# Optimization experiments

Measured on AMD Instinct MI355X. Metric: run time of the kernel, lower is better.

The kernel has to match this reference:

```python
import jax, jax.numpy as jnp
import numpy as np

B, L1, L2, C = 8, 2048, 2048, 320
H, D = 8, 64            # heads, dim_head -> inner_dim = 512
NREG = 4                # num_register_tokens
INNER = H * D
SCALE = D ** -0.5


def setup_inputs() -> dict:
    key = jax.random.key(0)
    ks = jax.random.split(key, 9)
    x = jax.random.normal(ks[0], (B, L1, C), dtype=jnp.float32)
    context = jax.random.normal(ks[1], (B, L2, C), dtype=jnp.float32)
    attn_mask = jax.random.randint(ks[2], (B, L1, L2), 0, 2).astype(bool)
    s = C ** -0.5
    Wq = jax.random.normal(ks[3], (C, INNER), dtype=jnp.float32) * s
    Wk = jax.random.normal(ks[4], (C, INNER), dtype=jnp.float32) * s
    Wv = jax.random.normal(ks[5], (C, INNER), dtype=jnp.float32) * s
    Wo = jax.random.normal(ks[6], (INNER, C), dtype=jnp.float32) * (INNER ** -0.5)
    bo = jnp.zeros((C,), dtype=jnp.float32)
    reg_tokens = jax.random.normal(ks[7], (1, NREG, C), dtype=jnp.float32)
    return {"x": x, "context": context, "attn_mask": attn_mask,
            "Wq": Wq, "Wk": Wk, "Wv": Wv, "Wo": Wo, "bo": bo,
            "reg_tokens": reg_tokens}


def reference(x, context, attn_mask, Wq, Wk, Wv, Wo, bo, reg_tokens):
    b = x.shape[0]
    # prepend register tokens to context: [B, NREG+L2, C]
    ctx = jnp.concatenate([jnp.broadcast_to(reg_tokens, (b, NREG, C)), context], axis=1)
    q = (x @ Wq).reshape(b, L1, H, D).transpose(0, 2, 1, 3)          # B H L1 D
    k = (ctx @ Wk).reshape(b, NREG + L2, H, D).transpose(0, 2, 1, 3)  # B H Lk D
    v = (ctx @ Wv).reshape(b, NREG + L2, H, D).transpose(0, 2, 1, 3)
    # pad mask with True for register tokens (always visible)
    mask = jnp.pad(attn_mask, ((0, 0), (0, 0), (NREG, 0)), constant_values=True)
    scores = jnp.einsum('bhqd,bhkd->bhqk', q, k) * SCALE              # B H L1 Lk
    scores = jnp.where(mask[:, None, :, :], scores, -jnp.inf)
    attn = jax.nn.softmax(scores, axis=-1)
    out = jnp.einsum('bhqk,bhkd->bhqd', attn, v)                      # B H L1 D
    out = out.transpose(0, 2, 1, 3).reshape(b, L1, INNER)             # B L1 (H D)
    return out @ Wo + bo
```

## Files before the change

kernel.cpp:

```cpp
#include <hip/hip_runtime.h>
#include <hip/hip_bf16.h>

#define B_ 8
#define L1_ 2048
#define L2_ 2048
#define C_ 320
#define H_ 8
#define D_ 64
#define NREG_ 4
#define INNER_ 512
#define LK_ 2052
#define LKP_ 2112
#define NKV_TILES 33
#define LOG2E 1.44269504f
#define QSCALE (0.125f * LOG2E)

typedef __bf16 bf16_t;
typedef __attribute__((ext_vector_type(8))) __bf16 bf16x8;
typedef __attribute__((ext_vector_type(4))) __bf16 bf16x4;
typedef __attribute__((ext_vector_type(4))) float f32x4;

__device__ __forceinline__ f32x4 mfma16(bf16x8 a, bf16x8 b, f32x4 c){
  return __builtin_amdgcn_mfma_f32_16x16x32_bf16(a, b, c, 0, 0, 0);
}

__device__ __forceinline__ void gl_lds16(const char* g, char* l){
  __builtin_amdgcn_global_load_lds(
      (const __attribute__((address_space(1))) unsigned int*)g,
      (__attribute__((address_space(3))) unsigned int*)l, 16, 0, 0);
}

__device__ __forceinline__ float fexp2(float x){
  float r; asm("v_exp_f32 %0, %1" : "=v"(r) : "v"(x)); return r;
}

__device__ __forceinline__ int swzK(int row){ return (row & 3) | ((row >> 1) & 4); }
__device__ __forceinline__ int swzV(int row){ return row & 7; }

__global__ void k_transpose(const float* __restrict__ Wq, const float* __restrict__ Wk,
                            const float* __restrict__ Wv, const float* __restrict__ Wo,
                            bf16_t* __restrict__ Wqt, bf16_t* __restrict__ Wkt,
                            bf16_t* __restrict__ Wvt, bf16_t* __restrict__ Wot){
  int z = blockIdx.z;
  int K = (z < 3) ? C_ : INNER_;
  int N = (z < 3) ? INNER_ : C_;
  if (blockIdx.x * 32 >= N || blockIdx.y * 32 >= K) return;
  const float* W = (z == 0) ? Wq : (z == 1) ? Wk : (z == 2) ? Wv : Wo;
  bf16_t* Wt = (z == 0) ? Wqt : (z == 1) ? Wkt : (z == 2) ? Wvt : Wot;
  float sc = (z == 0) ? QSCALE : 1.0f;
  __shared__ float t[32][33];
  int n0 = blockIdx.x * 32, k0 = blockIdx.y * 32;
  int tx = threadIdx.x & 31, ty = threadIdx.x >> 5;
  for (int r = ty; r < 32; r += 8) t[r][tx] = W[(long)(k0 + r) * N + n0 + tx];
  __syncthreads();
  for (int r = ty; r < 32; r += 8) Wt[(long)(n0 + r) * K + k0 + tx] = (bf16_t)(t[tx][r] * sc);
}

__global__ __launch_bounds__(256)
void k_cvt(const float* __restrict__ x, const float* __restrict__ ctx,
           const float* __restrict__ regt,
           bf16_t* __restrict__ xb, bf16_t* __restrict__ ctxb){
  long g = (long)blockIdx.x * 256 + threadIdx.x;
  if (blockIdx.y == 0){
    if (g >= (long)16384 * 80) return;
    f32x4 v = *(const f32x4*)(x + g * 4);
    bf16x4 cv;
    cv[0]=(bf16_t)v[0]; cv[1]=(bf16_t)v[1]; cv[2]=(bf16_t)v[2]; cv[3]=(bf16_t)v[3];
    *(bf16x4*)(xb + g * 4) = cv;
  } else {
    if (g >= (long)16896 * 80) return;
    long row = g / 80;
    int col = (int)(g - row * 80) * 4;
    int b = (int)(row / LKP_);
    int rr = (int)(row - (long)b * LKP_);
    f32x4 v = (f32x4){0,0,0,0};
    if (rr < NREG_)    v = *(const f32x4*)(regt + rr * C_ + col);
    else if (rr < LK_) v = *(const f32x4*)(ctx + ((long)(b * L1_ + rr - NREG_)) * C_ + col);
    bf16x4 cv;
    cv[0]=(bf16_t)v[0]; cv[1]=(bf16_t)v[1]; cv[2]=(bf16_t)v[2]; cv[3]=(bf16_t)v[3];
    *(bf16x4*)(ctxb + row * C_ + col) = cv;
  }
}

__global__ void k_maskcompact(const void* __restrict__ maskv,
                              unsigned int* __restrict__ maskp){
  int row = blockIdx.x * 4 + (threadIdx.x >> 6);
  int l = threadIdx.x & 63;
  const unsigned char* mb = (const unsigned char*)maskv;
  const int* mi = (const int*)maskv;
  int bad = 0;
  #pragma unroll
  for (int jj = 0; jj < 4; jj++){
    int j = l + jj * 64;
    if ((j & 3) != 0 && mb[j] != 0) bad = 1;
  }
  int isInt = (__ballot(bad) == 0ull) ? 1 : 0;
  unsigned int* orow = maskp + (long)row * 66;
  if (!isInt){
    const unsigned char* rp = mb + (long)row * L2_;
    unsigned wdv = 0;
    #pragma unroll
    for (int i = 0; i < 8; i++){
      unsigned u;
      if (l == 0 && i == 0) u = 0x01010101u;
      else u = *(const unsigned*)(rp + (32 * l - 4 + 4 * i));
      unsigned bits = 0;
      bits |= (u & 0x000000FFu) ? 1u : 0u;
      bits |= (u & 0x0000FF00u) ? 2u : 0u;
      bits |= (u & 0x00FF0000u) ? 4u : 0u;
      bits |= (u & 0xFF000000u) ? 8u : 0u;
      wdv |= bits << (4 * i);
    }
    orow[l] = wdv;
    if (l < 2){
      unsigned wd2 = 0;
      if (l == 0){
        unsigned u = *(const unsigned*)(rp + 2044);
        wd2 |= (u & 0x000000FFu) ? 1u : 0u;
        wd2 |= (u & 0x0000FF00u) ? 2u : 0u;
        wd2 |= (u & 0x00FF0000u) ? 4u : 0u;
        wd2 |= (u & 0xFF000000u) ? 8u : 0u;
      }
      orow[64 + l] = wd2;
    }
  } else {
    long base = (long)row * L2_;
    for (int s = 0; s < 33; s++){
      int kv = s * 64 + l;
      int vis = 0;
      if (kv < NREG_) vis = 1;
      else if (kv < LK_) vis = (mi[base + kv - NREG_] != 0);
      unsigned long long bal = __ballot(vis);
      if (l == 0)      orow[2*s]   = (unsigned int)bal;
      else if (l == 1) orow[2*s+1] = (unsigned int)(bal >> 32);
    }
  }
}

__global__ __launch_bounds__(256)
void k_proj(const bf16_t* __restrict__ xb, const bf16_t* __restrict__ ctxb,
            const bf16_t* __restrict__ Wqt, const bf16_t* __restrict__ Wkt,
            const bf16_t* __restrict__ Wvt,
            bf16_t* __restrict__ Qw, bf16_t* __restrict__ Kw, bf16_t* __restrict__ Vtw)
{
  int mode = blockIdx.z;
  if (mode == 0 && blockIdx.x >= 128) return;
  const char* Ab = (const char*)((mode == 0) ? xb : ctxb);
  const char* Wtb = (const char*)((mode == 0) ? Wqt : (mode == 1) ? Wkt : Wvt);
  bf16_t* out = (mode == 0) ? Qw : (mode == 1) ? Kw : Vtw;

  __shared__ __align__(16) char As[128*64*2];
  __shared__ __align__(16) char Bs[128*64*2];
  int tid = threadIdx.x;
  int w = tid >> 6, lane = tid & 63, cl = lane & 15, cg = lane >> 4;
  int wr = w >> 1, wc = w & 1;
  int m0 = blockIdx.x * 128, n0 = blockIdx.y * 128;

  f32x4 acc[4][4];
  #pragma unroll
  for (int i = 0; i < 4; i++)
    #pragma unroll
    for (int j = 0; j < 4; j++) acc[i][j] = (f32x4){0,0,0,0};

  for (int kb = 0; kb < 5; ++kb){
    __syncthreads();
    #pragma unroll
    for (int c = 0; c < 4; c++){
      int e = c * 4096 + tid * 16;
      int row = e >> 7, irb = e & 127;
      gl_lds16(Ab + (long)(m0 + row) * 640 + kb * 128 + (irb ^ ((row & 7) << 4)), As + e);
    }
    #pragma unroll
    for (int c = 0; c < 4; c++){
      int e = c * 4096 + tid * 16;
      int row = e >> 7, irb = e & 127;
      gl_lds16(Wtb + (long)(n0 + row) * 640 + kb * 128 + (irb ^ ((row & 7) << 4)), Bs + e);
    }
    asm volatile("s_waitcnt vmcnt(0)" ::: "memory");
    __syncthreads();
    #pragma unroll
    for (int kc = 0; kc < 2; kc++){
      int kk = kc * 32 + cg * 8;
      bf16x8 af[4], bfr[4];
      #pragma unroll
      for (int mt = 0; mt < 4; mt++){
        int row = wr * 64 + mt * 16 + cl;
        af[mt] = *(const bf16x8*)(As + (row << 7) + ((kk << 1) ^ ((row & 7) << 4)));
      }
      #pragma unroll
      for (int nt = 0; nt < 4; nt++){
        int row = wc * 64 + nt * 16 + cl;
        bfr[nt] = *(const bf16x8*)(Bs + (row << 7) + ((kk << 1) ^ ((row & 7) << 4)));
      }
      #pragma unroll
      for (int mt = 0; mt < 4; mt++)
        #pragma unroll
        for (int nt = 0; nt < 4; nt++)
          acc[mt][nt] = mfma16(af[mt], bfr[nt], acc[mt][nt]);
    }
  }

  #pragma unroll
  for (int mt = 0; mt < 4; mt++){
    #pragma unroll
    for (int nt = 0; nt < 4; nt++){
      f32x4 v = acc[mt][nt];
      int row = m0 + wr * 64 + mt * 16 + cg * 4;
      int col = n0 + wc * 64 + nt * 16 + cl;
      int h = col >> 6, d = col & 63;
      if (mode == 0){
        int b = row >> 11, l1 = row & 2047;
        bf16_t* p = out + ((long)((b * H_ + h) * L1_ + l1)) * D_ + d;
        #pragma unroll
        for (int r = 0; r < 4; r++) p[r * D_] = (bf16_t)v[r];
      } else if (mode == 1){
        int b = row / LKP_, rr = row - b * LKP_;
        bf16_t* p = out + ((long)((b * H_ + h) * LKP_ + rr)) * D_ + d;
        #pragma unroll
        for (int r = 0; r < 4; r++) p[r * D_] = (bf16_t)v[r];
      } else {
        int b = row / LKP_, rr = row - b * LKP_;
        bf16x4 cv;
        cv[0]=(bf16_t)v[0]; cv[1]=(bf16_t)v[1]; cv[2]=(bf16_t)v[2]; cv[3]=(bf16_t)v[3];
        *(bf16x4*)(out + ((long)((b * H_ + h) * D_ + d)) * LKP_ + rr) = cv;
      }
    }
  }
}

__global__ __launch_bounds__(512)
void k_attn(const bf16_t* __restrict__ Q, const bf16_t* __restrict__ K,
            const bf16_t* __restrict__ Vt, const unsigned int* __restrict__ maskp,
            bf16_t* __restrict__ att)
{
  __shared__ __align__(16) char smem[32768];
  int lin = blockIdx.x;
  int xcd = lin & 7, idx = lin >> 3;
  int bh = xcd * 8 + (idx >> 3);
  int qb = idx & 7;
  const int b = bh >> 3, h = bh & 7;
  const int tid = threadIdx.x, w = tid >> 6, lane = tid & 63;
  const int cl = lane & 15, cg = lane >> 4;
  const int qw = qb * 256 + w * 32;

  const char* Kg = (const char*)(K + (long)bh * LKP_ * D_);
  const char* Vg = (const char*)(Vt + (long)bh * D_ * LKP_);

  bf16x8 qf[2][2];
  const unsigned int* mrow[2];
  #pragma unroll
  for (int qg = 0; qg < 2; qg++){
    const bf16_t* Qb = Q + ((long)bh * L1_ + qw + qg*16 + cl) * D_;
    qf[qg][0] = *(const bf16x8*)(Qb + cg*8);
    qf[qg][1] = *(const bf16x8*)(Qb + 32 + cg*8);
    mrow[qg] = maskp + (long)(b * L1_ + qw + qg*16 + cl) * 66;
  }

  bf16x8 ones8;
  #pragma unroll
  for (int i = 0; i < 8; i++) ones8[i] = (bf16_t)1.0f;

  f32x4 o[2][4];
  f32x4 sacc[2];
  #pragma unroll
  for (int qg = 0; qg < 2; qg++){
    sacc[qg] = (f32x4){0,0,0,0};
    #pragma unroll
    for (int dt = 0; dt < 4; dt++) o[qg][dt] = (f32x4){0,0,0,0};
  }

  const int sp = tid * 16;
  const int srow = sp >> 7, sir = sp & 127;
  const int kgo = (srow << 7) + (sir ^ (swzK(srow) << 4));
  const long vgo = (long)srow * (LKP_ * 2) + (sir ^ (swzV(srow) << 4));

  gl_lds16(Kg + kgo, smem + sp);
  gl_lds16(Vg + vgo, smem + 16384 + sp);
  uint2 wd_cur[2];
  #pragma unroll
  for (int qg = 0; qg < 2; qg++) wd_cur[qg] = *(const uint2*)(mrow[qg]);
  asm volatile("s_waitcnt vmcnt(0)" ::: "memory");
  __syncthreads();

  for (int t = 0; t < NKV_TILES; ++t){
    int tn = (t + 1 < NKV_TILES) ? t + 1 : NKV_TILES - 1;
    gl_lds16(Kg + (long)tn * 8192 + kgo, smem + ((t + 1) & 1) * 8192 + sp);
    gl_lds16(Vg + vgo + tn * 128, smem + 16384 + ((t + 1) & 1) * 8192 + sp);
    uint2 wd_nxt[2];
    #pragma unroll
    for (int qg = 0; qg < 2; qg++) wd_nxt[qg] = *(const uint2*)(mrow[qg] + 2*tn);

    const char* Kb = smem + (t & 1) * 8192;
    const char* Vb = smem + 16384 + (t & 1) * 8192;

    f32x4 s[2][4];
    __builtin_amdgcn_s_setprio(1);
    #pragma unroll
    for (int T = 0; T < 4; T++){
      int row = 32*(T>>1) + 8*(cl>>2) + 4*(T&1) + (cl&3);
      int sw = swzK(row) << 4;
      const char* rp = Kb + (row << 7);
      bf16x8 kf0 = *(const bf16x8*)(rp + ((16*cg) ^ sw));
      bf16x8 kf1 = *(const bf16x8*)(rp + ((64 + 16*cg) ^ sw));
      #pragma unroll
      for (int qg = 0; qg < 2; qg++){
        f32x4 z = (f32x4){0,0,0,0};
        z = mfma16(kf0, qf[qg][0], z);
        z = mfma16(kf1, qf[qg][1], z);
        s[qg][T] = z;
      }
    }
    __builtin_amdgcn_s_setprio(0);

    bf16x8 pa[2][2];
    #pragma unroll
    for (int qg = 0; qg < 2; qg++){
      #pragma unroll
      for (int T = 0; T < 4; T++){
        unsigned wsel = (T < 2) ? wd_cur[qg].x : wd_cur[qg].y;
        unsigned nib = (wsel >> (8*cg + 4*(T&1))) & 0xFu;
        float p0 = fexp2(s[qg][T][0]);
        float p1 = fexp2(s[qg][T][1]);
        float p2 = fexp2(s[qg][T][2]);
        float p3 = fexp2(s[qg][T][3]);
        p0 = (nib & 1u) ? p0 : 0.f;
        p1 = (nib & 2u) ? p1 : 0.f;
        p2 = (nib & 4u) ? p2 : 0.f;
        p3 = (nib & 8u) ? p3 : 0.f;
        int a = T >> 1, jb = (T & 1) * 4;
        pa[qg][a][jb+0] = (bf16_t)p0;
        pa[qg][a][jb+1] = (bf16_t)p1;
        pa[qg][a][jb+2] = (bf16_t)p2;
        pa[qg][a][jb+3] = (bf16_t)p3;
      }
    }

    __builtin_amdgcn_s_setprio(1);
    #pragma unroll
    for (int qg = 0; qg < 2; qg++){
      sacc[qg] = mfma16(ones8, pa[qg][0], sacc[qg]);
      sacc[qg] = mfma16(ones8, pa[qg][1], sacc[qg]);
    }
    #pragma unroll
    for (int dt = 0; dt < 4; dt++){
      int row = 16*dt + cl;
      int sw = swzV(row) << 4;
      const char* rp = Vb + (row << 7);
      bf16x8 vf0 = *(const bf16x8*)(rp + ((16*cg) ^ sw));
      bf16x8 vf1 = *(const bf16x8*)(rp + ((64 + 16*cg) ^ sw));
      #pragma unroll
      for (int qg = 0; qg < 2; qg++){
        o[qg][dt] = mfma16(pa[qg][0], vf0, o[qg][dt]);
        o[qg][dt] = mfma16(pa[qg][1], vf1, o[qg][dt]);
      }
    }
    __builtin_amdgcn_s_setprio(0);

    asm volatile("s_waitcnt vmcnt(0)" ::: "memory");
    __syncthreads();
    wd_cur[0] = wd_nxt[0];
    wd_cur[1] = wd_nxt[1];
  }

  #pragma unroll
  for (int qg = 0; qg < 2; qg++){
    float inv = 1.0f / sacc[qg][0];
    float ir0 = __shfl(inv, (lane & 48) | (cg*4 + 0));
    float ir1 = __shfl(inv, (lane & 48) | (cg*4 + 1));
    float ir2 = __shfl(inv, (lane & 48) | (cg*4 + 2));
    float ir3 = __shfl(inv, (lane & 48) | (cg*4 + 3));
    int qbase = qw + qg*16 + cg*4;
    #pragma unroll
    for (int dt = 0; dt < 4; dt++){
      bf16_t* op = att + ((long)(b * L1_) + qbase) * INNER_ + h * D_ + 16*dt + cl;
      op[0] = (bf16_t)(o[qg][dt][0] * ir0);
      op[INNER_] = (bf16_t)(o[qg][dt][1] * ir1);
      op[2*INNER_] = (bf16_t)(o[qg][dt][2] * ir2);
      op[3*INNER_] = (bf16_t)(o[qg][dt][3] * ir3);
    }
  }
}

__global__ __launch_bounds__(256)
void k_out(const bf16_t* __restrict__ A, const bf16_t* __restrict__ Wot,
           const float* __restrict__ bo, float* __restrict__ out)
{
  __shared__ __align__(16) char As[128*64*2];
  __shared__ __align__(16) char Bs[64*64*2];
  int tid = threadIdx.x;
  int w = tid >> 6, lane = tid & 63, cl = lane & 15, cg = lane >> 4;
  int wr = w >> 1, wc = w & 1;
  int m0 = blockIdx.x * 128, n0 = blockIdx.y * 64;
  const char* Ab = (const char*)A;
  const char* Bb = (const char*)Wot;

  f32x4 acc[4][2];
  #pragma unroll
  for (int i = 0; i < 4; i++)
    #pragma unroll
    for (int j = 0; j < 2; j++) acc[i][j] = (f32x4){0,0,0,0};

  for (int kb = 0; kb < 8; kb++){
    __syncthreads();
    #pragma unroll
    for (int c = 0; c < 4; c++){
      int e = c * 4096 + tid * 16;
      int row = e >> 7, irb = e & 127;
      gl_lds16(Ab + (long)(m0 + row) * 1024 + kb * 128 + (irb ^ ((row & 7) << 4)), As + e);
    }
    #pragma unroll
    for (int c = 0; c < 2; c++){
      int e = c * 4096 + tid * 16;
      int row = e >> 7, irb = e & 127;
      gl_lds16(Bb + (long)(n0 + row) * 1024 + kb * 128 + (irb ^ ((row & 7) << 4)), Bs + e);
    }
    asm volatile("s_waitcnt vmcnt(0)" ::: "memory");
    __syncthreads();
    #pragma unroll
    for (int kc = 0; kc < 2; kc++){
      int kk = kc * 32 + cg * 8;
      bf16x8 af[4], bfr[2];
      #pragma unroll
      for (int mt = 0; mt < 4; mt++){
        int row = wr * 64 + mt * 16 + cl;
        af[mt] = *(const bf16x8*)(As + (row << 7) + ((kk << 1) ^ ((row & 7) << 4)));
      }
      #pragma unroll
      for (int nt = 0; nt < 2; nt++){
        int row = wc * 32 + nt * 16 + cl;
        bfr[nt] = *(const bf16x8*)(Bs + (row << 7) + ((kk << 1) ^ ((row & 7) << 4)));
      }
      #pragma unroll
      for (int mt = 0; mt < 4; mt++)
        #pragma unroll
        for (int nt = 0; nt < 2; nt++)
          acc[mt][nt] = mfma16(af[mt], bfr[nt], acc[mt][nt]);
    }
  }
  #pragma unroll
  for (int mt = 0; mt < 4; mt++)
    #pragma unroll
    for (int nt = 0; nt < 2; nt++){
      int row = m0 + wr * 64 + mt * 16 + cg * 4;
      int col = n0 + wc * 32 + nt * 16 + cl;
      float bias = bo[col];
      #pragma unroll
      for (int r = 0; r < 4; r++)
        out[(long)(row + r) * C_ + col] = acc[mt][nt][r] + bias;
    }
}

extern "C" void kernel_launch(void* const* d_in, const int* in_sizes, int n_in,
                              void* d_out, int out_size, void* d_ws, size_t ws_size,
                              hipStream_t stream)
{
  const float* x    = (const float*)d_in[0];
  const float* ctx  = (const float*)d_in[1];
  const void*  mask = d_in[2];
  const float* Wq   = (const float*)d_in[3];
  const float* Wk   = (const float*)d_in[4];
  const float* Wv   = (const float*)d_in[5];
  const float* Wo   = (const float*)d_in[6];
  const float* bo   = (const float*)d_in[7];
  const float* regt = (const float*)d_in[8];
  float* out = (float*)d_out;

  char* ws = (char*)d_ws;
  size_t off = 256;
  unsigned int* maskp = (unsigned int*)(ws + off);    off += (size_t)16384 * 66 * 4;
  bf16_t* Qw  = (bf16_t*)(ws + off);                  off += (size_t)B_*H_*L1_*D_*2;
  bf16_t* Kw  = (bf16_t*)(ws + off);                  off += (size_t)B_*H_*LKP_*D_*2;
  bf16_t* Vtw = (bf16_t*)(ws + off);                  off += (size_t)B_*H_*D_*LKP_*2;
  size_t Roff = off;
  bf16_t* xb   = (bf16_t*)(ws + Roff);
  bf16_t* ctxb = (bf16_t*)(ws + Roff + (size_t)16384*C_*2);
  bf16_t* Att  = (bf16_t*)(ws + Roff);
  off = Roff + (size_t)16384*C_*2 + (size_t)16896*C_*2;
  bf16_t* Wqt = (bf16_t*)(ws + off);                  off += (size_t)C_*INNER_*2;
  bf16_t* Wkt = (bf16_t*)(ws + off);                  off += (size_t)C_*INNER_*2;
  bf16_t* Wvt = (bf16_t*)(ws + off);                  off += (size_t)C_*INNER_*2;
  bf16_t* Wot = (bf16_t*)(ws + off);                  off += (size_t)C_*INNER_*2;
  (void)ws_size; (void)in_sizes; (void)n_in; (void)out_size;

  k_transpose<<<dim3(16,16,4), 256, 0, stream>>>(Wq, Wk, Wv, Wo, Wqt, Wkt, Wvt, Wot);
  k_cvt<<<dim3(5280,2), 256, 0, stream>>>(x, ctx, regt, xb, ctxb);
  k_maskcompact<<<4096, 256, 0, stream>>>(mask, maskp);
  k_proj<<<dim3(132,4,3), 256, 0, stream>>>(xb, ctxb, Wqt, Wkt, Wvt, Qw, Kw, Vtw);
  k_attn<<<512, 512, 0, stream>>>(Qw, Kw, Vtw, maskp, Att);
  k_out<<<dim3(128,5), 256, 0, stream>>>(Att, Wot, bo, out);
}
```

Measured before the change: 206.1 us.

## Fuse prep kernels into one launch and double-buffer projection GEMM loads

Merges the weight transpose, input conversion and mask compaction kernels into a single launch that dispatches on block index, removing two kernel launches and their inter-kernel gaps. The projection and output GEMMs now use double-buffered LDS: each iteration prefetches the next K tile with global_load_lds while computing on the current one, with partial vmcnt waits and an extra barrier. This doubles LDS use per block, which may lower occupancy, and the shared-memory transpose tile is now allocated for every block of the fused kernel.

```diff
diff --git a/kernel.cpp b/kernel.cpp
--- a/kernel.cpp
+++ b/kernel.cpp
@@ -37,102 +37,104 @@
 __device__ __forceinline__ int swzK(int row){ return (row & 3) | ((row >> 1) & 4); }
 __device__ __forceinline__ int swzV(int row){ return row & 7; }
 
-__global__ void k_transpose(const float* __restrict__ Wq, const float* __restrict__ Wk,
-                            const float* __restrict__ Wv, const float* __restrict__ Wo,
-                            bf16_t* __restrict__ Wqt, bf16_t* __restrict__ Wkt,
-                            bf16_t* __restrict__ Wvt, bf16_t* __restrict__ Wot){
-  int z = blockIdx.z;
-  int K = (z < 3) ? C_ : INNER_;
-  int N = (z < 3) ? INNER_ : C_;
-  if (blockIdx.x * 32 >= N || blockIdx.y * 32 >= K) return;
-  const float* W = (z == 0) ? Wq : (z == 1) ? Wk : (z == 2) ? Wv : Wo;
-  bf16_t* Wt = (z == 0) ? Wqt : (z == 1) ? Wkt : (z == 2) ? Wvt : Wot;
-  float sc = (z == 0) ? QSCALE : 1.0f;
-  __shared__ float t[32][33];
-  int n0 = blockIdx.x * 32, k0 = blockIdx.y * 32;
-  int tx = threadIdx.x & 31, ty = threadIdx.x >> 5;
-  for (int r = ty; r < 32; r += 8) t[r][tx] = W[(long)(k0 + r) * N + n0 + tx];
-  __syncthreads();
-  for (int r = ty; r < 32; r += 8) Wt[(long)(n0 + r) * K + k0 + tx] = (bf16_t)(t[tx][r] * sc);
-}
-
 __global__ __launch_bounds__(256)
-void k_cvt(const float* __restrict__ x, const float* __restrict__ ctx,
-           const float* __restrict__ regt,
-           bf16_t* __restrict__ xb, bf16_t* __restrict__ ctxb){
-  long g = (long)blockIdx.x * 256 + threadIdx.x;
-  if (blockIdx.y == 0){
-    if (g >= (long)16384 * 80) return;
-    f32x4 v = *(const f32x4*)(x + g * 4);
-    bf16x4 cv;
-    cv[0]=(bf16_t)v[0]; cv[1]=(bf16_t)v[1]; cv[2]=(bf16_t)v[2]; cv[3]=(bf16_t)v[3];
-    *(bf16x4*)(xb + g * 4) = cv;
+void k_prep(const float* __restrict__ Wq, const float* __restrict__ Wk,
+            const float* __restrict__ Wv, const float* __restrict__ Wo,
+            bf16_t* __restrict__ Wqt, bf16_t* __restrict__ Wkt,
+            bf16_t* __restrict__ Wvt, bf16_t* __restrict__ Wot,
+            const float* __restrict__ x, const float* __restrict__ ctx,
+            const float* __restrict__ regt,
+            bf16_t* __restrict__ xb, bf16_t* __restrict__ ctxb,
+            const void* __restrict__ maskv, unsigned int* __restrict__ maskp)
+{
+  int bid = blockIdx.x;
+  int tid = threadIdx.x;
+  if (bid < 1024){
+    int z = bid >> 8, r = bid & 255, bx = r & 15, by = r >> 4;
+    int K = (z < 3) ? C_ : INNER_;
+    int N = (z < 3) ? INNER_ : C_;
+    if (bx * 32 >= N || by * 32 >= K) return;
+    const float* W = (z == 0) ? Wq : (z == 1) ? Wk : (z == 2) ? Wv : Wo;
+    bf16_t* Wt = (z == 0) ? Wqt : (z == 1) ? Wkt : (z == 2) ? Wvt : Wot;
+    float sc = (z == 0) ? QSCALE : 1.0f;
+    __shared__ float t[32][33];
+    int n0 = bx * 32, k0 = by * 32;
+    int tx = tid & 31, ty = tid >> 5;
+    for (int rr = ty; rr < 32; rr += 8) t[rr][tx] = W[(long)(k0 + rr) * N + n0 + tx];
+    __syncthreads();
+    for (int rr = ty; rr < 32; rr += 8) Wt[(long)(n0 + rr) * K + k0 + tx] = (bf16_t)(t[tx][rr] * sc);
+  } else if (bid < 11424){
+    int b2 = bid - 1024;
+    if (b2 < 5120){
+      long g = (long)b2 * 256 + tid;
+      f32x4 v = *(const f32x4*)(x + g * 4);
+      bf16x4 cv;
+      cv[0]=(bf16_t)v[0]; cv[1]=(bf16_t)v[1]; cv[2]=(bf16_t)v[2]; cv[3]=(bf16_t)v[3];
+      *(bf16x4*)(xb + g * 4) = cv;
+    } else {
+      long g = (long)(b2 - 5120) * 256 + tid;
+      long row = g / 80;
+      int col = (int)(g - row * 80) * 4;
+      int b = (int)(row / LKP_);
+      int rr = (int)(row - (long)b * LKP_);
+      f32x4 v = (f32x4){0,0,0,0};
+      if (rr < NREG_)    v = *(const f32x4*)(regt + rr * C_ + col);
+      else if (rr < LK_) v = *(const f32x4*)(ctx + ((long)(b * L1_ + rr - NREG_)) * C_ + col);
+      bf16x4 cv;
+      cv[0]=(bf16_t)v[0]; cv[1]=(bf16_t)v[1]; cv[2]=(bf16_t)v[2]; cv[3]=(bf16_t)v[3];
+      *(bf16x4*)(ctxb + row * C_ + col) = cv;
+    }
   } else {
-    if (g >= (long)16896 * 80) return;
-    long row = g / 80;
-    int col = (int)(g - row * 80) * 4;
-    int b = (int)(row / LKP_);
-    int rr = (int)(row - (long)b * LKP_);
-    f32x4 v = (f32x4){0,0,0,0};
-    if (rr < NREG_)    v = *(const f32x4*)(regt + rr * C_ + col);
-    else if (rr < LK_) v = *(const f32x4*)(ctx + ((long)(b * L1_ + rr - NREG_)) * C_ + col);
-    bf16x4 cv;
-    cv[0]=(bf16_t)v[0]; cv[1]=(bf16_t)v[1]; cv[2]=(bf16_t)v[2]; cv[3]=(bf16_t)v[3];
-    *(bf16x4*)(ctxb + row * C_ + col) = cv;
-  }
-}
-
-__global__ void k_maskcompact(const void* __restrict__ maskv,
-                              unsigned int* __restrict__ maskp){
-  int row = blockIdx.x * 4 + (threadIdx.x >> 6);
-  int l = threadIdx.x & 63;
-  const unsigned char* mb = (const unsigned char*)maskv;
-  const int* mi = (const int*)maskv;
-  int bad = 0;
-  #pragma unroll
-  for (int jj = 0; jj < 4; jj++){
-    int j = l + jj * 64;
-    if ((j & 3) != 0 && mb[j] != 0) bad = 1;
-  }
-  int isInt = (__ballot(bad) == 0ull) ? 1 : 0;
-  unsigned int* orow = maskp + (long)row * 66;
-  if (!isInt){
-    const unsigned char* rp = mb + (long)row * L2_;
-    unsigned wdv = 0;
-    #pragma unroll
-    for (int i = 0; i < 8; i++){
-      unsigned u;
-      if (l == 0 && i == 0) u = 0x01010101u;
-      else u = *(const unsigned*)(rp + (32 * l - 4 + 4 * i));
-      unsigned bits = 0;
-      bits |= (u & 0x000000FFu) ? 1u : 0u;
-      bits |= (u & 0x0000FF00u) ? 2u : 0u;
-      bits |= (u & 0x00FF0000u) ? 4u : 0u;
-      bits |= (u & 0xFF000000u) ? 8u : 0u;
-      wdv |= bits << (4 * i);
-    }
-    orow[l] = wdv;
-    if (l < 2){
-      unsigned wd2 = 0;
-      if (l == 0){
-        unsigned u = *(const unsigned*)(rp + 2044);
-        wd2 |= (u & 0x000000FFu) ? 1u : 0u;
-        wd2 |= (u & 0x0000FF00u) ? 2u : 0u;
-        wd2 |= (u & 0x00FF0000u) ? 4u : 0u;
-        wd2 |= (u & 0xFF000000u) ? 8u : 0u;
-      }
-      orow[64 + l] = wd2;
-    }
-  } else {
-    long base = (long)row * L2_;
-    for (int s = 0; s < 33; s++){
-      int kv = s * 64 + l;
-      int vis = 0;
-      if (kv < NREG_) vis = 1;
-      else if (kv < LK_) vis = (mi[base + kv - NREG_] != 0);
-      unsigned long long bal = __ballot(vis);
-      if (l == 0)      orow[2*s]   = (unsigned int)bal;
-      else if (l == 1) orow[2*s+1] = (unsigned int)(bal >> 32);
+    int row = (bid - 11424) * 4 + (tid >> 6);
+    int l = tid & 63;
+    const unsigned char* mb = (const unsigned char*)maskv;
+    const int* mi = (const int*)maskv;
+    int bad = 0;
+    #pragma unroll
+    for (int jj = 0; jj < 4; jj++){
+      int j = l + jj * 64;
+      if ((j & 3) != 0 && mb[j] != 0) bad = 1;
+    }
+    int isInt = (__ballot(bad) == 0ull) ? 1 : 0;
+    unsigned int* orow = maskp + (long)row * 66;
+    if (!isInt){
+      const unsigned char* rp = mb + (long)row * L2_;
+      unsigned wdv = 0;
+      #pragma unroll
+      for (int i = 0; i < 8; i++){
+        unsigned u;
+        if (l == 0 && i == 0) u = 0x01010101u;
+        else u = *(const unsigned*)(rp + (32 * l - 4 + 4 * i));
+        unsigned bits = 0;
+        bits |= (u & 0x000000FFu) ? 1u : 0u;
+        bits |= (u & 0x0000FF00u) ? 2u : 0u;
+        bits |= (u & 0x00FF0000u) ? 4u : 0u;
+        bits |= (u & 0xFF000000u) ? 8u : 0u;
+        wdv |= bits << (4 * i);
+      }
+      orow[l] = wdv;
+      if (l < 2){
+        unsigned wd2 = 0;
+        if (l == 0){
+          unsigned u = *(const unsigned*)(rp + 2044);
+          wd2 |= (u & 0x000000FFu) ? 1u : 0u;
+          wd2 |= (u & 0x0000FF00u) ? 2u : 0u;
+          wd2 |= (u & 0x00FF0000u) ? 4u : 0u;
+          wd2 |= (u & 0xFF000000u) ? 8u : 0u;
+        }
+        orow[64 + l] = wd2;
+      }
+    } else {
+      long base = (long)row * L2_;
+      for (int s = 0; s < 33; s++){
+        int kv = s * 64 + l;
+        int vis = 0;
+        if (kv < NREG_) vis = 1;
+        else if (kv < LK_) vis = (mi[base + kv - NREG_] != 0);
+        unsigned long long bal = __ballot(vis);
+        if (l == 0)      orow[2*s]   = (unsigned int)bal;
+        else if (l == 1) orow[2*s+1] = (unsigned int)(bal >> 32);
+      }
     }
   }
 }
@@ -149,8 +151,8 @@
   const char* Wtb = (const char*)((mode == 0) ? Wqt : (mode == 1) ? Wkt : Wvt);
   bf16_t* out = (mode == 0) ? Qw : (mode == 1) ? Kw : Vtw;
 
-  __shared__ __align__(16) char As[128*64*2];
-  __shared__ __align__(16) char Bs[128*64*2];
+  __shared__ __align__(16) char As[2][128*64*2];
+  __shared__ __align__(16) char Bs[2][128*64*2];
   int tid = threadIdx.x;
   int w = tid >> 6, lane = tid & 63, cl = lane & 15, cg = lane >> 4;
   int wr = w >> 1, wc = w & 1;
@@ -162,21 +164,30 @@
     #pragma unroll
     for (int j = 0; j < 4; j++) acc[i][j] = (f32x4){0,0,0,0};
 
-  for (int kb = 0; kb < 5; ++kb){
-    __syncthreads();
+  auto stage = [&](int kb, int buf){
     #pragma unroll
     for (int c = 0; c < 4; c++){
       int e = c * 4096 + tid * 16;
       int row = e >> 7, irb = e & 127;
-      gl_lds16(Ab + (long)(m0 + row) * 640 + kb * 128 + (irb ^ ((row & 7) << 4)), As + e);
+      gl_lds16(Ab + (long)(m0 + row) * 640 + kb * 128 + (irb ^ ((row & 7) << 4)), As[buf] + e);
     }
     #pragma unroll
     for (int c = 0; c < 4; c++){
       int e = c * 4096 + tid * 16;
       int row = e >> 7, irb = e & 127;
-      gl_lds16(Wtb + (long)(n0 + row) * 640 + kb * 128 + (irb ^ ((row & 7) << 4)), Bs + e);
-    }
-    asm volatile("s_waitcnt vmcnt(0)" ::: "memory");
+      gl_lds16(Wtb + (long)(n0 + row) * 640 + kb * 128 + (irb ^ ((row & 7) << 4)), Bs[buf] + e);
+    }
+  };
+
+  stage(0, 0);
+  for (int kb = 0; kb < 5; ++kb){
+    int buf = kb & 1;
+    if (kb < 4){
+      stage(kb + 1, buf ^ 1);
+      asm volatile("s_waitcnt vmcnt(8)" ::: "memory");
+    } else {
+      asm volatile("s_waitcnt vmcnt(0)" ::: "memory");
+    }
     __syncthreads();
     #pragma unroll
     for (int kc = 0; kc < 2; kc++){
@@ -185,12 +196,12 @@
       #pragma unroll
       for (int mt = 0; mt < 4; mt++){
         int row = wr * 64 + mt * 16 + cl;
-        af[mt] = *(const bf16x8*)(As + (row << 7) + ((kk << 1) ^ ((row & 7) << 4)));
+        af[mt] = *(const bf16x8*)(As[buf] + (row << 7) + ((kk << 1) ^ ((row & 7) << 4)));
       }
       #pragma unroll
       for (int nt = 0; nt < 4; nt++){
         int row = wc * 64 + nt * 16 + cl;
-        bfr[nt] = *(const bf16x8*)(Bs + (row << 7) + ((kk << 1) ^ ((row & 7) << 4)));
+        bfr[nt] = *(const bf16x8*)(Bs[buf] + (row << 7) + ((kk << 1) ^ ((row & 7) << 4)));
       }
       #pragma unroll
       for (int mt = 0; mt < 4; mt++)
@@ -198,6 +209,7 @@
         for (int nt = 0; nt < 4; nt++)
           acc[mt][nt] = mfma16(af[mt], bfr[nt], acc[mt][nt]);
     }
+    __syncthreads();
   }
 
   #pragma unroll
@@ -385,8 +397,8 @@
 void k_out(const bf16_t* __restrict__ A, const bf16_t* __restrict__ Wot,
            const float* __restrict__ bo, float* __restrict__ out)
 {
-  __shared__ __align__(16) char As[128*64*2];
-  __shared__ __align__(16) char Bs[64*64*2];
+  __shared__ __align__(16) char As[2][128*64*2];
+  __shared__ __align__(16) char Bs[2][64*64*2];
   int tid = threadIdx.x;
   int w = tid >> 6, lane = tid & 63, cl = lane & 15, cg = lane >> 4;
   int wr = w >> 1, wc = w & 1;
@@ -400,21 +412,30 @@
     #pragma unroll
     for (int j = 0; j < 2; j++) acc[i][j] = (f32x4){0,0,0,0};
 
-  for (int kb = 0; kb < 8; kb++){
-    __syncthreads();
+  auto stage = [&](int kb, int buf){
     #pragma unroll
     for (int c = 0; c < 4; c++){
       int e = c * 4096 + tid * 16;
       int row = e >> 7, irb = e & 127;
-      gl_lds16(Ab + (long)(m0 + row) * 1024 + kb * 128 + (irb ^ ((row & 7) << 4)), As + e);
+      gl_lds16(Ab + (long)(m0 + row) * 1024 + kb * 128 + (irb ^ ((row & 7) << 4)), As[buf] + e);
     }
     #pragma unroll
     for (int c = 0; c < 2; c++){
       int e = c * 4096 + tid * 16;
       int row = e >> 7, irb = e & 127;
-      gl_lds16(Bb + (long)(n0 + row) * 1024 + kb * 128 + (irb ^ ((row & 7) << 4)), Bs + e);
-    }
-    asm volatile("s_waitcnt vmcnt(0)" ::: "memory");
+      gl_lds16(Bb + (long)(n0 + row) * 1024 + kb * 128 + (irb ^ ((row & 7) << 4)), Bs[buf] + e);
+    }
+  };
+
+  stage(0, 0);
+  for (int kb = 0; kb < 8; kb++){
+    int buf = kb & 1;
+    if (kb < 7){
+      stage(kb + 1, buf ^ 1);
+      asm volatile("s_waitcnt vmcnt(6)" ::: "memory");
+    } else {
+      asm volatile("s_waitcnt vmcnt(0)" ::: "memory");
+    }
     __syncthreads();
     #pragma unroll
     for (int kc = 0; kc < 2; kc++){
@@ -423,12 +444,12 @@
       #pragma unroll
       for (int mt = 0; mt < 4; mt++){
         int row = wr * 64 + mt * 16 + cl;
-        af[mt] = *(const bf16x8*)(As + (row << 7) + ((kk << 1) ^ ((row & 7) << 4)));
+        af[mt] = *(const bf16x8*)(As[buf] + (row << 7) + ((kk << 1) ^ ((row & 7) << 4)));
       }
       #pragma unroll
       for (int nt = 0; nt < 2; nt++){
         int row = wc * 32 + nt * 16 + cl;
-        bfr[nt] = *(const bf16x8*)(Bs + (row << 7) + ((kk << 1) ^ ((row & 7) << 4)));
+        bfr[nt] = *(const bf16x8*)(Bs[buf] + (row << 7) + ((kk << 1) ^ ((row & 7) << 4)));
       }
       #pragma unroll
       for (int mt = 0; mt < 4; mt++)
@@ -436,6 +457,7 @@
         for (int nt = 0; nt < 2; nt++)
           acc[mt][nt] = mfma16(af[mt], bfr[nt], acc[mt][nt]);
     }
+    __syncthreads();
   }
   #pragma unroll
   for (int mt = 0; mt < 4; mt++)
@@ -482,9 +504,8 @@
   bf16_t* Wot = (bf16_t*)(ws + off);                  off += (size_t)C_*INNER_*2;
   (void)ws_size; (void)in_sizes; (void)n_in; (void)out_size;
 
-  k_transpose<<<dim3(16,16,4), 256, 0, stream>>>(Wq, Wk, Wv, Wo, Wqt, Wkt, Wvt, Wot);
-  k_cvt<<<dim3(5280,2), 256, 0, stream>>>(x, ctx, regt, xb, ctxb);
-  k_maskcompact<<<4096, 256, 0, stream>>>(mask, maskp);
+  k_prep<<<15520, 256, 0, stream>>>(Wq, Wk, Wv, Wo, Wqt, Wkt, Wvt, Wot,
+                                    x, ctx, regt, xb, ctxb, mask, maskp);
   k_proj<<<dim3(132,4,3), 256, 0, stream>>>(xb, ctxb, Wqt, Wkt, Wvt, Qw, Kw, Vtw);
   k_attn<<<512, 512, 0, stream>>>(Qw, Kw, Vtw, maskp, Att);
   k_out<<<dim3(128,5), 256, 0, stream>>>(Att, Wot, bo, out);
```

Result: faster. 197.8 us (-4.0%).
